# Kernel optimization log

Hardware: AMD Instinct MI355X
Metric: run time of the kernel (lower is better)

Reference implementation:

```python
import jax, jax.numpy as jnp
import numpy as np

PAD_BIG = 1e20  # matches F.pad(value=1e20) on y2


def setup_inputs() -> dict:
    key = jax.random.key(0)
    k1, k2, k3 = jax.random.split(key, 3)
    N, C, H, W = 2, 256, 96, 96
    x = jax.random.normal(k1, (N, C, H, W), dtype=jnp.float32)
    y = jax.random.normal(k2, (N, C, H, W), dtype=jnp.float32)
    labels = jax.random.randint(k3, (N, 1, H, W), 0, 124, dtype=jnp.int32)
    return {"x": x, "y": y, "labels": labels, "max_distance": 4, "num_class": 124}


def _window_stack(p, md, h, w):
    # p: padded [n, c, h+2*md, w+2*md] -> [n, c, h, w, k*k]; offset order
    # (di-major, dj-minor) matches F.unfold column ordering.
    k = 2 * md + 1
    return jnp.stack(
        [p[:, :, di:di + h, dj:dj + w] for di in range(k) for dj in range(k)],
        axis=-1,
    )


def reference(x, y, labels, max_distance, num_class):
    # x: query embedding [N,C,H,W]; y: prev-frame embedding [N,C,H,W]
    # labels: prev-frame labels [N,1,H,W] int
    n, c, h, w = x.shape
    md = max_distance
    k = 2 * md + 1
    kk = k * k

    x2 = jnp.sum(x * x, axis=1)  # [n,h,w]
    y2 = jnp.sum(y * y, axis=1, keepdims=True)  # [n,1,h,w]

    pad_sp = [(0, 0), (0, 0), (md, md), (md, md)]
    py = jnp.pad(y, pad_sp)                                   # zeros
    py2 = jnp.pad(y2, pad_sp, constant_values=PAD_BIG)
    plab = jnp.pad(labels.astype(jnp.float32), pad_sp, constant_values=-1.0)

    y_off = _window_stack(py, md, h, w)          # [n,c,h,w,kk]
    y2_off = _window_stack(py2, md, h, w)[:, 0]  # [n,h,w,kk]
    lab_off = _window_stack(plab, md, h, w)[:, 0]  # [n,h,w,kk]

    corr = jnp.einsum('nchw,nchwp->nhwp', x, y_off)  # [n,h,w,kk]
    d = x2[..., None] + y2_off - 2.0 * corr
    d = (jax.nn.sigmoid(d) - 0.5) * 2.0              # in (-1, 1)

    gt_ids = jnp.arange(num_class, dtype=jnp.float32)
    # mask: [n,h,w,kk,num_class]; padded label -1 never matches -> fill 1.0
    mask = lab_off[..., None] == gt_ids
    dists = jnp.min(jnp.where(mask, d[..., None], 1.0), axis=3)  # [n,h,w,nc]
    return jnp.transpose(dists, (0, 3, 1, 2))  # [n,num_class,h,w]
```

## Files before the change

kernel.cpp:

```cpp
#include <hip/hip_runtime.h>

#define Nn 2
#define Cc 256
#define Hh 96
#define Ww 96
#define HW (Hh * Ww)
#define MD 4
#define NC 124
#define TH 4
#define TWD 8
#define NQ (TH * TWD)
#define SH (TH + 2 * MD)
#define SWD (TWD + 2 * MD)
#define NS (SH * SWD)
#define BLK 256
#define KC 32
#define NCH (Cc / KC)
#define NBW (Ww / TWD)
#define NBH (Hh / TH)
#define NBLK (Nn * NBH * NBW)
#define YROW 64
#define XOFF (NS * YROW)
#define BUFSZ (XOFF + NQ * YROW)
#define TBL (NQ * NC)

typedef short short8 __attribute__((ext_vector_type(8)));
typedef float f32x4 __attribute__((ext_vector_type(4)));

__device__ __forceinline__ unsigned fmap(float f) {
    unsigned b = __float_as_uint(f);
    return (b & 0x80000000u) ? ~b : (b | 0x80000000u);
}
__device__ __forceinline__ float funmap(unsigned u) {
    unsigned b = (u & 0x80000000u) ? (u & 0x7fffffffu) : ~u;
    return __uint_as_float(b);
}
__device__ __forceinline__ int swz(int row, int slot) {
    return row * YROW + ((slot ^ ((row >> 1) & 3)) << 4);
}

__global__ __launch_bounds__(BLK) void propnet_mfma(
    const float* __restrict__ x, const float* __restrict__ y,
    const int* __restrict__ labels, float* __restrict__ out)
{
    __shared__ __align__(16) unsigned char sbuf[2][BUFSZ];
    __shared__ float y2s[NS];
    __shared__ float x2s[NQ];
    __shared__ int   labs[NS];
    unsigned* table = (unsigned*)&sbuf[0][0];

    const int t = threadIdx.x;

    const int orig = blockIdx.x;
    const int lin  = (orig & 7) * (NBLK / 8) + (orig >> 3);
    const int n    = lin / (NBH * NBW);
    const int rem  = lin - n * (NBH * NBW);
    const int h0   = (rem / NBW) * TH;
    const int w0   = (rem % NBW) * TWD;
    const size_t nb = (size_t)n * Cc * HW;

    if (t < NS) {
        y2s[t] = 0.f;
        const int sr = t >> 4, sc = t & 15;
        const int gh = h0 - MD + sr, gw = w0 - MD + sc;
        const bool ok = (gh >= 0) && (gh < Hh) && (gw >= 0) && (gw < Ww);
        labs[t] = ok ? labels[(size_t)n * HW + gh * Ww + gw] : -1;
    }
    if (t < NQ) x2s[t] = 0.f;

    const float* yptr[3]; int yoff[3]; int ypix[3];
#pragma unroll
    for (int i = 0; i < 3; ++i) {
        const int task = t + BLK * i;
        const int pix  = task % NS;
        const int grp  = task / NS;
        const int sr = pix >> 4, sc = pix & 15;
        const int gh = min(max(h0 - MD + sr, 0), Hh - 1);
        const int gw = min(max(w0 - MD + sc, 0), Ww - 1);
        yptr[i] = y + nb + (size_t)(grp * 8) * HW + (size_t)gh * Ww + gw;
        yoff[i] = swz(pix, grp);
        ypix[i] = pix;
    }
    const float* xptr = x; int xoffw = 0, xpix = 0;
    if (t < 128) {
        xpix = t & 31;
        const int grp = t >> 5;
        const int qr = xpix >> 3, qc = xpix & 7;
        xptr = x + nb + (size_t)(grp * 8) * HW + (size_t)(h0 + qr) * Ww + (w0 + qc);
        xoffw = XOFF + swz(xpix, grp);
    }
    float ysq[3] = {0.f, 0.f, 0.f};
    float xsq = 0.f;

    auto stage = [&](unsigned char* bb, int c) {
        const size_t coff = (size_t)c * (KC * HW);
#pragma unroll
        for (int i = 0; i < 3; ++i) {
            const float* p = yptr[i] + coff;
            float v[8];
#pragma unroll
            for (int j = 0; j < 8; ++j) v[j] = p[(size_t)j * HW];
            unsigned pk[4];
#pragma unroll
            for (int j = 0; j < 4; ++j) {
                ysq[i] = fmaf(v[2*j],   v[2*j],   ysq[i]);
                ysq[i] = fmaf(v[2*j+1], v[2*j+1], ysq[i]);
                pk[j] = (__float_as_uint(v[2*j]) >> 16) |
                        (__float_as_uint(v[2*j+1]) & 0xffff0000u);
            }
            *(uint4*)(bb + yoff[i]) = make_uint4(pk[0], pk[1], pk[2], pk[3]);
        }
        if (t < 128) {
            const float* p = xptr + coff;
            float v[8];
#pragma unroll
            for (int j = 0; j < 8; ++j) v[j] = p[(size_t)j * HW];
            unsigned pk[4];
#pragma unroll
            for (int j = 0; j < 4; ++j) {
                xsq = fmaf(v[2*j],   v[2*j],   xsq);
                xsq = fmaf(v[2*j+1], v[2*j+1], xsq);
                pk[j] = (__float_as_uint(v[2*j]) >> 16) |
                        (__float_as_uint(v[2*j+1]) & 0xffff0000u);
            }
            *(uint4*)(bb + xoffw) = make_uint4(pk[0], pk[1], pk[2], pk[3]);
        }
    };

    const int lane = t & 63;
    const int wid  = t >> 6;
    const int l15  = lane & 15;
    const int lg   = lane >> 4;
    int aoff[2], boff[3];
#pragma unroll
    for (int mf = 0; mf < 2; ++mf) aoff[mf] = XOFF + swz(mf * 16 + l15, lg);
#pragma unroll
    for (int nf = 0; nf < 3; ++nf) boff[nf] = swz(wid * 48 + nf * 16 + l15, lg);

    f32x4 acc[2][3];
#pragma unroll
    for (int mf = 0; mf < 2; ++mf)
#pragma unroll
        for (int nf = 0; nf < 3; ++nf)
            acc[mf][nf] = (f32x4){0.f, 0.f, 0.f, 0.f};

    auto compute = [&](const unsigned char* bb) {
        short8 a[2], b[3];
#pragma unroll
        for (int mf = 0; mf < 2; ++mf) a[mf] = *(const short8*)(bb + aoff[mf]);
#pragma unroll
        for (int nf = 0; nf < 3; ++nf) b[nf] = *(const short8*)(bb + boff[nf]);
#pragma unroll
        for (int mf = 0; mf < 2; ++mf)
#pragma unroll
            for (int nf = 0; nf < 3; ++nf)
                acc[mf][nf] = __builtin_amdgcn_mfma_f32_16x16x32_bf16(
                    a[mf], b[nf], acc[mf][nf], 0, 0, 0);
    };

    stage(sbuf[0], 0);
    __syncthreads();
    for (int cc = 0; cc < 4; ++cc) {
        stage(sbuf[1], 2 * cc + 1);
        compute(sbuf[0]);
        __syncthreads();
        if (cc < 3) stage(sbuf[0], 2 * cc + 2);
        compute(sbuf[1]);
        __syncthreads();
    }

#pragma unroll
    for (int i = 0; i < 3; ++i) atomicAdd(&y2s[ypix[i]], ysq[i]);
    if (t < 128) atomicAdd(&x2s[xpix], xsq);
    for (int i = t; i < TBL; i += BLK) table[i] = 0xBF800000u;
    __syncthreads();

#pragma unroll
    for (int mf = 0; mf < 2; ++mf) {
#pragma unroll
        for (int nf = 0; nf < 3; ++nf) {
#pragma unroll
            for (int r = 0; r < 4; ++r) {
                const int q = mf * 16 + lg * 4 + r;
                const int s = wid * 48 + nf * 16 + l15;
                const int qr = q >> 3, qc = q & 7;
                const int sr = s >> 4, sc = s & 15;
                const int di = sr - qr, dj = sc - qc;
                const int lab = labs[s];
                if (di >= 0 && di <= 2 * MD && dj >= 0 && dj <= 2 * MD &&
                    lab >= 0 && lab < NC) {
                    const float d  = x2s[q] + y2s[s] - 2.0f * acc[mf][nf][r];
                    const float sg = 1.0f / (1.0f + __expf(-d));
                    atomicMin(&table[q * NC + lab], fmap(fmaf(2.0f, sg, -1.0f)));
                }
            }
        }
    }
    __syncthreads();

    const size_t ob = (size_t)n * NC * HW;
    for (int i = t; i < TBL; i += BLK) {
        const int g = i >> 5;
        const int q = i & 31;
        const int qr = q >> 3, qc = q & 7;
        out[ob + (size_t)g * HW + (size_t)(h0 + qr) * Ww + (w0 + qc)] =
            funmap(table[q * NC + g]);
    }
}

extern "C" void kernel_launch(void* const* d_in, const int* in_sizes, int n_in,
                              void* d_out, int out_size, void* d_ws, size_t ws_size,
                              hipStream_t stream) {
    const float* x      = (const float*)d_in[0];
    const float* y      = (const float*)d_in[1];
    const int*   labels = (const int*)d_in[2];
    float*       out    = (float*)d_out;
    (void)in_sizes; (void)n_in; (void)out_size; (void)d_ws; (void)ws_size;

    propnet_mfma<<<dim3(NBLK), dim3(BLK), 0, stream>>>(x, y, labels, out);
}
```

Before: 31.68 us.

## Pre-pack y into bf16 channel-interleaved layout and stage via direct global-to-LDS loads

Adds a prep kernel that converts y once into packed bf16 groups of 8 channels per pixel and computes ||y||^2 into workspace, so the main kernel no longer re-reads each y halo pixel as fp32 strided loads and re-converts it in every tile. The main kernel stages y with global_load_lds 16-byte transfers straight into swizzled shared memory and splits x staging into a load and a write phase around compute. This adds two extra launches (memset and prep) plus a workspace round trip, and uses atomics for the y2 partial sums.

```diff
diff --git a/kernel.cpp b/kernel.cpp
--- a/kernel.cpp
+++ b/kernel.cpp
@@ -1,4 +1,5 @@
 #include <hip/hip_runtime.h>
+#include <stdint.h>
 
 #define Nn 2
 #define Cc 256
@@ -14,8 +15,6 @@
 #define SWD (TWD + 2 * MD)
 #define NS (SH * SWD)
 #define BLK 256
-#define KC 32
-#define NCH (Cc / KC)
 #define NBW (Ww / TWD)
 #define NBH (Hh / TH)
 #define NBLK (Nn * NBH * NBW)
@@ -23,6 +22,15 @@
 #define XOFF (NS * YROW)
 #define BUFSZ (XOFF + NQ * YROW)
 #define TBL (NQ * NC)
+#define CQ 32
+
+#define PSTRIP 16
+#define PPIX (HW / PSTRIP)
+#define PBLK (Nn * CQ * PSTRIP)
+
+#define YT_U4   ((size_t)Nn * CQ * HW)
+#define Y2_OFF  (YT_U4 * 16)
+#define Y2_BYTES ((size_t)Nn * HW * 4)
 
 typedef short short8 __attribute__((ext_vector_type(8)));
 typedef float f32x4 __attribute__((ext_vector_type(4)));
@@ -39,9 +47,47 @@
     return row * YROW + ((slot ^ ((row >> 1) & 3)) << 4);
 }
 
+__global__ __launch_bounds__(256) void prep_y(
+    const float* __restrict__ y, uint4* __restrict__ yT, float* __restrict__ y2g)
+{
+    __shared__ float tile[8 * PPIX];
+    const int t = threadIdx.x;
+    const int bid = blockIdx.x;
+    const int n = bid / (CQ * PSTRIP);
+    const int r = bid - n * (CQ * PSTRIP);
+    const int cq = r / PSTRIP;
+    const int strip = r - cq * PSTRIP;
+    const size_t pbase = (size_t)strip * PPIX;
+    const float* src = y + ((size_t)n * Cc + cq * 8) * HW + pbase;
+
+    for (int task = t; task < 8 * (PPIX / 4); task += 256) {
+        const int ch = task / (PPIX / 4);
+        const int p4 = task - ch * (PPIX / 4);
+        const float4 v = *(const float4*)(src + (size_t)ch * HW + p4 * 4);
+        *(float4*)&tile[ch * PPIX + p4 * 4] = v;
+    }
+    __syncthreads();
+
+    uint4* dst = yT + ((size_t)n * CQ + cq) * HW + pbase;
+    float* y2p = y2g + (size_t)n * HW + pbase;
+    for (int p = t; p < PPIX; p += 256) {
+        float v[8]; float sq = 0.f;
+#pragma unroll
+        for (int c = 0; c < 8; ++c) { v[c] = tile[c * PPIX + p]; sq = fmaf(v[c], v[c], sq); }
+        uint4 pk;
+        pk.x = (__float_as_uint(v[0]) >> 16) | (__float_as_uint(v[1]) & 0xffff0000u);
+        pk.y = (__float_as_uint(v[2]) >> 16) | (__float_as_uint(v[3]) & 0xffff0000u);
+        pk.z = (__float_as_uint(v[4]) >> 16) | (__float_as_uint(v[5]) & 0xffff0000u);
+        pk.w = (__float_as_uint(v[6]) >> 16) | (__float_as_uint(v[7]) & 0xffff0000u);
+        dst[p] = pk;
+        atomicAdd(&y2p[p], sq);
+    }
+}
+
 __global__ __launch_bounds__(BLK) void propnet_mfma(
-    const float* __restrict__ x, const float* __restrict__ y,
-    const int* __restrict__ labels, float* __restrict__ out)
+    const float* __restrict__ x, const uint4* __restrict__ yT,
+    const float* __restrict__ y2g, const int* __restrict__ labels,
+    float* __restrict__ out)
 {
     __shared__ __align__(16) unsigned char sbuf[2][BUFSZ];
     __shared__ float y2s[NS];
@@ -57,80 +103,78 @@
     const int rem  = lin - n * (NBH * NBW);
     const int h0   = (rem / NBW) * TH;
     const int w0   = (rem % NBW) * TWD;
-    const size_t nb = (size_t)n * Cc * HW;
 
     if (t < NS) {
-        y2s[t] = 0.f;
         const int sr = t >> 4, sc = t & 15;
         const int gh = h0 - MD + sr, gw = w0 - MD + sc;
         const bool ok = (gh >= 0) && (gh < Hh) && (gw >= 0) && (gw < Ww);
         labs[t] = ok ? labels[(size_t)n * HW + gh * Ww + gw] : -1;
+        y2s[t]  = ok ? y2g[(size_t)n * HW + gh * Ww + gw] : 0.f;
     }
     if (t < NQ) x2s[t] = 0.f;
 
-    const float* yptr[3]; int yoff[3]; int ypix[3];
-#pragma unroll
-    for (int i = 0; i < 3; ++i) {
-        const int task = t + BLK * i;
-        const int pix  = task % NS;
-        const int grp  = task / NS;
-        const int sr = pix >> 4, sc = pix & 15;
-        const int gh = min(max(h0 - MD + sr, 0), Hh - 1);
-        const int gw = min(max(w0 - MD + sc, 0), Ww - 1);
-        yptr[i] = y + nb + (size_t)(grp * 8) * HW + (size_t)gh * Ww + gw;
-        yoff[i] = swz(pix, grp);
-        ypix[i] = pix;
-    }
+    const int lane = t & 63;
+    const int wid  = t >> 6;
+
+    size_t ysrc[3]; int yl[3];
+    {
+        const int sc4 = lane >> 2;
+        const int pos = lane & 3;
+        const int cqw = pos ^ ((sc4 >> 1) & 3);
+#pragma unroll
+        for (int i = 0; i < 3; ++i) {
+            const int g  = wid * 3 + i;
+            const int gh = min(max(h0 - MD + g, 0), Hh - 1);
+            const int gw = min(max(w0 - MD + sc4, 0), Ww - 1);
+            ysrc[i] = (size_t)cqw * HW + (size_t)gh * Ww + gw;
+            yl[i]   = g * 1024;
+        }
+    }
+    const uint4* yTn = yT + (size_t)n * CQ * HW;
+    auto stageY = [&](int b, int c) {
+        const uint4* base = yTn + (size_t)(c * 4) * HW;
+#pragma unroll
+        for (int i = 0; i < 3; ++i) {
+            const void* gp = (const void*)(base + ysrc[i]);
+            void*       lp = (void*)(sbuf[b] + yl[i]);
+            __builtin_amdgcn_global_load_lds(
+                (const __attribute__((address_space(1))) unsigned int*)gp,
+                (__attribute__((address_space(3))) unsigned int*)lp, 16, 0, 0);
+        }
+    };
+
+    const bool xw = (t < 128);
     const float* xptr = x; int xoffw = 0, xpix = 0;
-    if (t < 128) {
+    if (xw) {
         xpix = t & 31;
         const int grp = t >> 5;
         const int qr = xpix >> 3, qc = xpix & 7;
-        xptr = x + nb + (size_t)(grp * 8) * HW + (size_t)(h0 + qr) * Ww + (w0 + qc);
+        xptr = x + ((size_t)n * Cc + grp * 8) * HW + (size_t)(h0 + qr) * Ww + (w0 + qc);
         xoffw = XOFF + swz(xpix, grp);
     }
-    float ysq[3] = {0.f, 0.f, 0.f};
     float xsq = 0.f;
-
-    auto stage = [&](unsigned char* bb, int c) {
-        const size_t coff = (size_t)c * (KC * HW);
-#pragma unroll
-        for (int i = 0; i < 3; ++i) {
-            const float* p = yptr[i] + coff;
-            float v[8];
-#pragma unroll
-            for (int j = 0; j < 8; ++j) v[j] = p[(size_t)j * HW];
-            unsigned pk[4];
-#pragma unroll
-            for (int j = 0; j < 4; ++j) {
-                ysq[i] = fmaf(v[2*j],   v[2*j],   ysq[i]);
-                ysq[i] = fmaf(v[2*j+1], v[2*j+1], ysq[i]);
-                pk[j] = (__float_as_uint(v[2*j]) >> 16) |
-                        (__float_as_uint(v[2*j+1]) & 0xffff0000u);
-            }
-            *(uint4*)(bb + yoff[i]) = make_uint4(pk[0], pk[1], pk[2], pk[3]);
-        }
-        if (t < 128) {
-            const float* p = xptr + coff;
-            float v[8];
-#pragma unroll
-            for (int j = 0; j < 8; ++j) v[j] = p[(size_t)j * HW];
-            unsigned pk[4];
-#pragma unroll
-            for (int j = 0; j < 4; ++j) {
-                xsq = fmaf(v[2*j],   v[2*j],   xsq);
-                xsq = fmaf(v[2*j+1], v[2*j+1], xsq);
-                pk[j] = (__float_as_uint(v[2*j]) >> 16) |
-                        (__float_as_uint(v[2*j+1]) & 0xffff0000u);
-            }
-            *(uint4*)(bb + xoffw) = make_uint4(pk[0], pk[1], pk[2], pk[3]);
-        }
-    };
-
-    const int lane = t & 63;
-    const int wid  = t >> 6;
-    const int l15  = lane & 15;
-    const int lg   = lane >> 4;
+    float xv[8];
+    auto xload = [&](int c) {
+        if (!xw) return;
+        const float* p = xptr + (size_t)(c * 32) * HW;
+#pragma unroll
+        for (int j = 0; j < 8; ++j) xv[j] = p[(size_t)j * HW];
+    };
+    auto xwrite = [&](int b) {
+        if (!xw) return;
+        unsigned pk[4];
+#pragma unroll
+        for (int j = 0; j < 4; ++j) {
+            xsq = fmaf(xv[2*j],   xv[2*j],   xsq);
+            xsq = fmaf(xv[2*j+1], xv[2*j+1], xsq);
+            pk[j] = (__float_as_uint(xv[2*j]) >> 16) |
+                    (__float_as_uint(xv[2*j+1]) & 0xffff0000u);
+        }
+        *(uint4*)(sbuf[b] + xoffw) = make_uint4(pk[0], pk[1], pk[2], pk[3]);
+    };
+
+    const int l15 = lane & 15;
+    const int lg  = lane >> 4;
     int aoff[2], boff[3];
 #pragma unroll
     for (int mf = 0; mf < 2; ++mf) aoff[mf] = XOFF + swz(mf * 16 + l15, lg);
@@ -158,20 +202,17 @@
                     a[mf], b[nf], acc[mf][nf], 0, 0, 0);
     };
 
-    stage(sbuf[0], 0);
-    __syncthreads();
-    for (int cc = 0; cc < 4; ++cc) {
-        stage(sbuf[1], 2 * cc + 1);
-        compute(sbuf[0]);
+    xload(0); stageY(0, 0); xwrite(0);
+    __syncthreads();
+    for (int c = 0; c < 8; ++c) {
+        const int b = c & 1;
+        if (c < 7) { xload(c + 1); stageY(b ^ 1, c + 1); }
+        compute(sbuf[b]);
+        if (c < 7) xwrite(b ^ 1);
         __syncthreads();
-        if (cc < 3) stage(sbuf[0], 2 * cc + 2);
-        compute(sbuf[1]);
-        __syncthreads();
-    }
-
-#pragma unroll
-    for (int i = 0; i < 3; ++i) atomicAdd(&y2s[ypix[i]], ysq[i]);
-    if (t < 128) atomicAdd(&x2s[xpix], xsq);
+    }
+
+    if (xw) atomicAdd(&x2s[xpix], xsq);
     for (int i = t; i < TBL; i += BLK) table[i] = 0xBF800000u;
     __syncthreads();
 
@@ -215,7 +256,11 @@
     const float* y      = (const float*)d_in[1];
     const int*   labels = (const int*)d_in[2];
     float*       out    = (float*)d_out;
-    (void)in_sizes; (void)n_in; (void)out_size; (void)d_ws; (void)ws_size;
-
-    propnet_mfma<<<dim3(NBLK), dim3(BLK), 0, stream>>>(x, y, labels, out);
-}
+    uint4* yT  = (uint4*)d_ws;
+    float* y2g = (float*)((char*)d_ws + Y2_OFF);
+    (void)in_sizes; (void)n_in; (void)out_size; (void)ws_size;
+
+    hipMemsetAsync(y2g, 0, Y2_BYTES, stream);
+    prep_y<<<dim3(PBLK), dim3(256), 0, stream>>>(y, yT, y2g);
+    propnet_mfma<<<dim3(NBLK), dim3(BLK), 0, stream>>>(x, yT, y2g, labels, out);
+}
```

Measured after the change: 37.29 us. 1.18x slower.

## Stage y halo via float4 row loads into fp32 LDS before bf16 packing

Applied to the files above, without the earlier changes.

Replaces the per-pixel strided scalar global loads of the y halo with coalesced float4 row-segment loads into an fp32 LDS staging buffer. Each thread then reads 8 channels from LDS and packs them into the swizzled bf16 MFMA buffer. The double-buffered bf16 tile becomes a single buffer, and each chunk iteration gains an extra barrier and an LDS round-trip. Register prefetch of the next chunk overlaps the global loads with compute. This trades higher LDS usage (a 32-channel fp32 tile), which may lower occupancy, for better global memory coalescing.

```diff
diff --git a/kernel.cpp b/kernel.cpp
--- a/kernel.cpp
+++ b/kernel.cpp
@@ -1,4 +1,5 @@
 #include <hip/hip_runtime.h>
+#include <stdint.h>
 
 #define Nn 2
 #define Cc 256
@@ -14,8 +15,6 @@
 #define SWD (TWD + 2 * MD)
 #define NS (SH * SWD)
 #define BLK 256
-#define KC 32
-#define NCH (Cc / KC)
 #define NBW (Ww / TWD)
 #define NBH (Hh / TH)
 #define NBLK (Nn * NBH * NBW)
@@ -39,15 +38,16 @@
     return row * YROW + ((slot ^ ((row >> 1) & 3)) << 4);
 }
 
-__global__ __launch_bounds__(BLK) void propnet_mfma(
+__global__ __launch_bounds__(BLK) void propnet_fused(
     const float* __restrict__ x, const float* __restrict__ y,
     const int* __restrict__ labels, float* __restrict__ out)
 {
-    __shared__ __align__(16) unsigned char sbuf[2][BUFSZ];
+    __shared__ __align__(16) float F[32 * NS];
+    __shared__ __align__(16) unsigned char B[BUFSZ];
     __shared__ float y2s[NS];
     __shared__ float x2s[NQ];
     __shared__ int   labs[NS];
-    unsigned* table = (unsigned*)&sbuf[0][0];
+    unsigned* table = (unsigned*)F;
 
     const int t = threadIdx.x;
 
@@ -60,46 +60,55 @@
     const size_t nb = (size_t)n * Cc * HW;
 
     if (t < NS) {
-        y2s[t] = 0.f;
         const int sr = t >> 4, sc = t & 15;
         const int gh = h0 - MD + sr, gw = w0 - MD + sc;
         const bool ok = (gh >= 0) && (gh < Hh) && (gw >= 0) && (gw < Ww);
         labs[t] = ok ? labels[(size_t)n * HW + gh * Ww + gw] : -1;
+        y2s[t]  = 0.f;
     }
     if (t < NQ) x2s[t] = 0.f;
 
-    const float* yptr[3]; int yoff[3]; int ypix[3];
+    const float* ysrc6[6]; int fwb[6];
+#pragma unroll
+    for (int k = 0; k < 6; ++k) {
+        const int task = t + 256 * k;
+        const int ch = task / 48;
+        const int r  = task - ch * 48;
+        const int g  = r >> 2;
+        const int sg = r & 3;
+        const int gh = min(max(h0 - MD + g, 0), Hh - 1);
+        const int ws = min(max(w0 - MD + sg * 4, 0), Ww - 4);
+        ysrc6[k] = y + nb + (size_t)ch * HW + (size_t)gh * Ww + ws;
+        fwb[k]   = ch * (NS * 4) + g * 64 + sg * 16;
+    }
+    float4 yv[6];
+    auto yload = [&](int c) {
+        const size_t coff = (size_t)(c * 32) * HW;
+#pragma unroll
+        for (int k = 0; k < 6; ++k) yv[k] = *(const float4*)(ysrc6[k] + coff);
+    };
+    auto fwrite = [&]() {
+#pragma unroll
+        for (int k = 0; k < 6; ++k) *(float4*)((char*)F + fwb[k]) = yv[k];
+    };
+
+    int ppix[3], pwb[3]; const float* pcol[3];
 #pragma unroll
     for (int i = 0; i < 3; ++i) {
-        const int task = t + BLK * i;
+        const int task = t + 256 * i;
         const int pix  = task % NS;
-        const int grp  = task / NS;
-        const int sr = pix >> 4, sc = pix & 15;
-        const int gh = min(max(h0 - MD + sr, 0), Hh - 1);
-        const int gw = min(max(w0 - MD + sc, 0), Ww - 1);
-        yptr[i] = y + nb + (size_t)(grp * 8) * HW + (size_t)gh * Ww + gw;
-        yoff[i] = swz(pix, grp);
-        ypix[i] = pix;
-    }
-    const float* xptr = x; int xoffw = 0, xpix = 0;
-    if (t < 128) {
-        xpix = t & 31;
-        const int grp = t >> 5;
-        const int qr = xpix >> 3, qc = xpix & 7;
-        xptr = x + nb + (size_t)(grp * 8) * HW + (size_t)(h0 + qr) * Ww + (w0 + qc);
-        xoffw = XOFF + swz(xpix, grp);
+        const int slot = task / NS;
+        ppix[i] = pix;
+        pwb[i]  = swz(pix, slot);
+        pcol[i] = F + slot * 8 * NS + pix;
     }
     float ysq[3] = {0.f, 0.f, 0.f};
-    float xsq = 0.f;
-
-    auto stage = [&](unsigned char* bb, int c) {
-        const size_t coff = (size_t)c * (KC * HW);
+    auto packY = [&]() {
 #pragma unroll
         for (int i = 0; i < 3; ++i) {
-            const float* p = yptr[i] + coff;
             float v[8];
 #pragma unroll
-            for (int j = 0; j < 8; ++j) v[j] = p[(size_t)j * HW];
+            for (int j = 0; j < 8; ++j) v[j] = pcol[i][j * NS];
             unsigned pk[4];
 #pragma unroll
             for (int j = 0; j < 4; ++j) {
@@ -108,23 +117,38 @@
                 pk[j] = (__float_as_uint(v[2*j]) >> 16) |
                         (__float_as_uint(v[2*j+1]) & 0xffff0000u);
             }
-            *(uint4*)(bb + yoff[i]) = make_uint4(pk[0], pk[1], pk[2], pk[3]);
+            *(uint4*)(B + pwb[i]) = make_uint4(pk[0], pk[1], pk[2], pk[3]);
         }
-        if (t < 128) {
-            const float* p = xptr + coff;
-            float v[8];
-#pragma unroll
-            for (int j = 0; j < 8; ++j) v[j] = p[(size_t)j * HW];
-            unsigned pk[4];
-#pragma unroll
-            for (int j = 0; j < 4; ++j) {
-                xsq = fmaf(v[2*j],   v[2*j],   xsq);
-                xsq = fmaf(v[2*j+1], v[2*j+1], xsq);
-                pk[j] = (__float_as_uint(v[2*j]) >> 16) |
-                        (__float_as_uint(v[2*j+1]) & 0xffff0000u);
-            }
-            *(uint4*)(bb + xoffw) = make_uint4(pk[0], pk[1], pk[2], pk[3]);
+    };
+
+    const bool xw = (t < 128);
+    const float* xptr = x; int xoffw = 0, xpix = 0;
+    if (xw) {
+        xpix = t & 31;
+        const int grp = t >> 5;
+        const int qr = xpix >> 3, qc = xpix & 7;
+        xptr = x + nb + (size_t)(grp * 8) * HW + (size_t)(h0 + qr) * Ww + (w0 + qc);
+        xoffw = XOFF + swz(xpix, grp);
+    }
+    float xsq = 0.f;
+    float xv[8];
+    auto xload = [&](int c) {
+        if (!xw) return;
+        const float* p = xptr + (size_t)(c * 32) * HW;
+#pragma unroll
+        for (int j = 0; j < 8; ++j) xv[j] = p[(size_t)j * HW];
+    };
+    auto xwrite = [&]() {
+        if (!xw) return;
+        unsigned pk[4];
+#pragma unroll
+        for (int j = 0; j < 4; ++j) {
+            xsq = fmaf(xv[2*j],   xv[2*j],   xsq);
+            xsq = fmaf(xv[2*j+1], xv[2*j+1], xsq);
+            pk[j] = (__float_as_uint(xv[2*j]) >> 16) |
+                    (__float_as_uint(xv[2*j+1]) & 0xffff0000u);
         }
+        *(uint4*)(B + xoffw) = make_uint4(pk[0], pk[1], pk[2], pk[3]);
     };
 
     const int lane = t & 63;
@@ -144,12 +168,12 @@
         for (int nf = 0; nf < 3; ++nf)
             acc[mf][nf] = (f32x4){0.f, 0.f, 0.f, 0.f};
 
-    auto compute = [&](const unsigned char* bb) {
+    auto compute = [&]() {
         short8 a[2], b[3];
 #pragma unroll
-        for (int mf = 0; mf < 2; ++mf) a[mf] = *(const short8*)(bb + aoff[mf]);
-#pragma unroll
-        for (int nf = 0; nf < 3; ++nf) b[nf] = *(const short8*)(bb + boff[nf]);
+        for (int mf = 0; mf < 2; ++mf) a[mf] = *(const short8*)(B + aoff[mf]);
+#pragma unroll
+        for (int nf = 0; nf < 3; ++nf) b[nf] = *(const short8*)(B + boff[nf]);
 #pragma unroll
         for (int mf = 0; mf < 2; ++mf)
 #pragma unroll
@@ -158,20 +182,23 @@
                     a[mf], b[nf], acc[mf][nf], 0, 0, 0);
     };
 
-    stage(sbuf[0], 0);
-    __syncthreads();
-    for (int cc = 0; cc < 4; ++cc) {
-        stage(sbuf[1], 2 * cc + 1);
-        compute(sbuf[0]);
+    yload(0); xload(0);
+    fwrite();
+    __syncthreads();
+    packY(); xwrite();
+    __syncthreads();
+    for (int c = 0; c < 8; ++c) {
+        if (c < 7) { yload(c + 1); xload(c + 1); }
+        compute();
+        if (c < 7) fwrite();
         __syncthreads();
-        if (cc < 3) stage(sbuf[0], 2 * cc + 2);
-        compute(sbuf[1]);
+        if (c < 7) { packY(); xwrite(); }
         __syncthreads();
     }
 
 #pragma unroll
-    for (int i = 0; i < 3; ++i) atomicAdd(&y2s[ypix[i]], ysq[i]);
-    if (t < 128) atomicAdd(&x2s[xpix], xsq);
+    for (int i = 0; i < 3; ++i) atomicAdd(&y2s[ppix[i]], ysq[i]);
+    if (xw) atomicAdd(&x2s[xpix], xsq);
     for (int i = t; i < TBL; i += BLK) table[i] = 0xBF800000u;
     __syncthreads();
 
@@ -217,5 +244,5 @@
     float*       out    = (float*)d_out;
     (void)in_sizes; (void)n_in; (void)out_size; (void)d_ws; (void)ws_size;
 
-    propnet_mfma<<<dim3(NBLK), dim3(BLK), 0, stream>>>(x, y, labels, out);
-}
+    propnet_fused<<<dim3(NBLK), dim3(BLK), 0, stream>>>(x, y, labels, out);
+}
```

Measured after the change: 55.88 us. 76.4% more time.
